# Kernel tuning notes

Hardware: AMD Instinct MI355X
Metric: run time of the kernel (lower is better)

## Reference

```python
import jax, jax.numpy as jnp
import numpy as np

B, T, C = 128, 64, 66
S, L, W = 512, 2, 32  # state_size, num_layers, window_size


def _gru_cell(x, h, Wih, Whh, bih, bhh):
    # PyTorch GRU cell. x:[B,in], h:[B,S]; gate order r,z,n.
    gi = x @ Wih.T + bih  # [B,3S]
    gh = h @ Whh.T + bhh
    ir, iz, inn = jnp.split(gi, 3, axis=-1)
    hr, hz, hn = jnp.split(gh, 3, axis=-1)
    r = jax.nn.sigmoid(ir + hr)
    z = jax.nn.sigmoid(iz + hz)
    n = jnp.tanh(inn + r * hn)
    return (1.0 - z) * n + z * h


def setup_inputs() -> dict:
    key = jax.random.key(0)
    ks = jax.random.split(key, 14)
    sc = 0.02
    inp = {
        'x': jax.random.normal(ks[0], (B, T, C), dtype=jnp.float32),
        'Wih0': jax.random.normal(ks[1], (3 * S, C), dtype=jnp.float32) * sc,
        'Whh0': jax.random.normal(ks[2], (3 * S, S), dtype=jnp.float32) * sc,
        'bih0': jax.random.normal(ks[3], (3 * S,), dtype=jnp.float32) * sc,
        'bhh0': jax.random.normal(ks[4], (3 * S,), dtype=jnp.float32) * sc,
        'Wih1': jax.random.normal(ks[5], (3 * S, S), dtype=jnp.float32) * sc,
        'Whh1': jax.random.normal(ks[6], (3 * S, S), dtype=jnp.float32) * sc,
        'bih1': jax.random.normal(ks[7], (3 * S,), dtype=jnp.float32) * sc,
        'bhh1': jax.random.normal(ks[8], (3 * S,), dtype=jnp.float32) * sc,
        'Wt': jax.random.normal(ks[9], (1, W), dtype=jnp.float32) * sc,   # temporal_fc_last: Linear(W,1)
        'bt': jnp.zeros((1,), dtype=jnp.float32),
        'Ws': jax.random.normal(ks[10], (C, S), dtype=jnp.float32) * sc,  # spatial_fc: Linear(S,C)
        'bs': jnp.zeros((C,), dtype=jnp.float32),
    }
    return inp


def reference(x, Wih0, Whh0, bih0, bhh0, Wih1, Whh1, bih1, bhh1, Wt, bt, Ws, bs):
    Bx, Tx, Cx = x.shape
    h0 = jnp.zeros((Bx, S), dtype=x.dtype)
    h1 = jnp.zeros((Bx, S), dtype=x.dtype)

    def stack_step(h0, h1, xt):
        h0 = _gru_cell(xt, h0, Wih0, Whh0, bih0, bhh0)
        h1 = _gru_cell(h0, h1, Wih1, Whh1, bih1, bhh1)
        return h0, h1

    # ---- encoder over x[:, :-1, :] ----
    def enc_step(carry, xt):
        h0, h1 = stack_step(carry[0], carry[1], xt)
        return (h0, h1), h1

    (h0, h1), enc_out = jax.lax.scan(enc_step, (h0, h1), x[:, :-1, :].transpose(1, 0, 2))
    # enc_out: [T-1, B, S]; sliding window of the last W encoder outputs: [B, W, S]
    window = enc_out[-W:].transpose(1, 0, 2)

    def dec_step(carry, _):
        h0, h1, win, dinp = carry  # dinp: [B, C]
        h0, h1 = stack_step(h0, h1, dinp)
        win = jnp.concatenate([win[:, 1:, :], h1[:, None, :]], axis=1)  # slide window
        # temporal_fc_last over time axis (after b n d -> b d n): [B, S]
        temp = jnp.einsum('bws,w->bs', win, Wt[0]) + bt[0]
        out = temp @ Ws.T + bs  # spatial_fc: [B, C]
        new_frame = out + dinp  # recursive residual
        return (h0, h1, win, new_frame), new_frame

    init = (h0, h1, window, x[:, -1, :])
    _, frames = jax.lax.scan(dec_step, init, None, length=Tx)  # [T, B, C]
    return frames.transpose(1, 0, 2)  # [B, T, C]
```

## Files before the change

kernel.cpp:

```cpp
#include <hip/hip_runtime.h>
#include <stdint.h>

typedef unsigned short u16;
typedef uint32_t u32;
typedef __attribute__((ext_vector_type(8))) short short8;
typedef __attribute__((ext_vector_type(4))) float floatx4;

constexpr int BB = 128;
constexpr int TT = 64;
constexpr int CC = 66;
constexpr int CPAD = 96;
constexpr int SS = 512;
constexpr int NGATE = 1536;
constexpr int NGRP = 8;
constexpr int GBLK = 16;
constexpr int GS = 16 * SS;


__device__ __forceinline__ u16 f2bf(float f) {
    u32 u = __float_as_uint(f);
    u32 r = (u + 0x7fffu + ((u >> 16) & 1u)) >> 16;
    return (u16)r;
}
__device__ __forceinline__ float bf2f(u16 h) {
    return __uint_as_float(((u32)h) << 16);
}
__device__ __forceinline__ float sigm(float x) { return 1.f / (1.f + __expf(-x)); }
__device__ __forceinline__ float tanh_f(float x) { return 1.f - 2.f / (1.f + __expf(2.f * x)); }

__device__ __forceinline__ void store_u16_cc(u16* p, u16 v) {
    asm volatile("global_store_short %0, %1, off sc0 sc1"
                 :: "v"(p), "v"((u32)v) : "memory");
}
__device__ __forceinline__ void load_issue_cc(const u16* p, short8& d) {
    asm volatile("global_load_dwordx4 %0, %1, off sc0 sc1"
                 : "=v"(d) : "v"(p));
}
__device__ __forceinline__ void vm_drain() {
    asm volatile("s_waitcnt vmcnt(0)" ::: "memory");
}

__global__ void prep1_kernel(const float* __restrict__ x,
                             const float* __restrict__ Wih0,
                             const float* __restrict__ Whh0,
                             const float* __restrict__ Wih1,
                             const float* __restrict__ Whh1,
                             const float* __restrict__ Ws,
                             u16* __restrict__ xbf, u16* __restrict__ wi0,
                             u16* __restrict__ wh0, u16* __restrict__ wi1,
                             u16* __restrict__ wh1, u16* __restrict__ wsb)
{
    const int N_xbf = BB * TT * CPAD;
    const int N_wi0 = NGATE * CPAD;
    const int N_whh = NGATE * SS;
    const int N_wsb = 80 * SS;
    const long total = (long)N_xbf + N_wi0 + 3L * N_whh + N_wsb;
    for (long i = (long)blockIdx.x * blockDim.x + threadIdx.x; i < total;
         i += (long)gridDim.x * blockDim.x) {
        long idx = i;
        if (idx < N_xbf) {
            int c = idx % CPAD; int bt = idx / CPAD;
            float v = (c < CC) ? x[(long)bt * CC + c] : 0.f;
            xbf[idx] = f2bf(v); continue;
        }
        idx -= N_xbf;
        if (idx < N_wi0) {
            int c = idx % CPAD; int n = idx / CPAD;
            float v = (c < CC) ? Wih0[(long)n * CC + c] : 0.f;
            wi0[idx] = f2bf(v); continue;
        }
        idx -= N_wi0;
        if (idx < N_whh) { wh0[idx] = f2bf(Whh0[idx]); continue; }
        idx -= N_whh;
        if (idx < N_whh) { wi1[idx] = f2bf(Wih1[idx]); continue; }
        idx -= N_whh;
        if (idx < N_whh) { wh1[idx] = f2bf(Whh1[idx]); continue; }
        idx -= N_whh;
        {
            int s = idx % SS; int c = idx / SS;
            wsb[idx] = (c < CC) ? f2bf(Ws[(long)c * SS + s]) : (u16)0;
        }
    }
}

__global__ void prep2_kernel(const float* __restrict__ x,
                             const float* __restrict__ Wih0,
                             const float* __restrict__ Ws,
                             const float* __restrict__ bs,
                             u16* __restrict__ Mbf, float* __restrict__ c0vec,
                             float* __restrict__ gi0i)
{
    const long NM = (long)NGATE * SS;
    const long NC = NGATE;
    const long NG = (long)BB * NGATE;
    const long total = NM + NC + NG;
    for (long i = (long)blockIdx.x * blockDim.x + threadIdx.x; i < total;
         i += (long)gridDim.x * blockDim.x) {
        long idx = i;
        if (idx < NM) {
            int s = idx % SS; int g = idx / SS;
            float acc = 0.f;
            for (int c = 0; c < CC; ++c)
                acc += Wih0[(long)g * CC + c] * Ws[(long)c * SS + s];
            Mbf[idx] = f2bf(acc); continue;
        }
        idx -= NM;
        if (idx < NC) {
            int g = idx;
            float acc = 0.f;
            for (int c = 0; c < CC; ++c) acc += Wih0[(long)g * CC + c] * bs[c];
            c0vec[g] = acc; continue;
        }
        idx -= NC;
        {
            int g = idx % NGATE; int b = idx / NGATE;
            float acc = 0.f;
            const float* xl = x + ((long)b * TT + (TT - 1)) * CC;
            for (int c = 0; c < CC; ++c) acc += xl[c] * Wih0[(long)g * CC + c];
            gi0i[idx] = acc;
        }
    }
}

__device__ __forceinline__ void load_afrags(const u16* __restrict__ st,
                                            int lane, short8* a) {
#pragma unroll
    for (int kc = 0; kc < 16; ++kc)
        load_issue_cc(st + (long)kc * 512 + lane * 8, a[kc]);
}

#define MFMA_BF16(a, wp, acc) \
    acc = __builtin_amdgcn_mfma_f32_16x16x32_bf16(a, *(const short8*)(wp), acc, 0, 0, 0)

__device__ __forceinline__ void mm3_reg(const short8* a,
                                        const u16* __restrict__ w0,
                                        const u16* __restrict__ w1,
                                        const u16* __restrict__ w2,
                                        floatx4& A0, floatx4& A1, floatx4& A2) {
#pragma unroll
    for (int kc = 0; kc < 16; ++kc) {
        const int k = kc << 5;
        MFMA_BF16(a[kc], w0 + k, A0);
        MFMA_BF16(a[kc], w1 + k, A1);
        MFMA_BF16(a[kc], w2 + k, A2);
    }
}

template <int K>
__device__ __forceinline__ void mm3_g(const u16* __restrict__ aP,
                                      const u16* __restrict__ w0,
                                      const u16* __restrict__ w1,
                                      const u16* __restrict__ w2,
                                      floatx4& A0, floatx4& A1, floatx4& A2) {
#pragma unroll
    for (int k = 0; k < K; k += 32) {
        short8 a = *(const short8*)(aP + k);
        MFMA_BF16(a, w0 + k, A0);
        MFMA_BF16(a, w1 + k, A1);
        MFMA_BF16(a, w2 + k, A2);
    }
}

__device__ __forceinline__ void wait2(const int* __restrict__ f0, int t0,
                                      const int* __restrict__ f1, int t1) {
    const int lane = threadIdx.x & 63;
    const int* p = (lane < 32) ? (f0 + lane) : (f1 + (lane - 32));
    const int tgt = (lane < 32) ? t0 : t1;
    for (;;) {
        int v = __hip_atomic_load(p, __ATOMIC_RELAXED, __HIP_MEMORY_SCOPE_AGENT);
        if (__all(v >= tgt)) break;
        __builtin_amdgcn_s_sleep(1);
    }
    asm volatile("" ::: "memory");
}

__device__ __forceinline__ void set_flag(int* f, int v) {
    if ((threadIdx.x & 63) == 0)
        __hip_atomic_store(f, v, __ATOMIC_RELAXED, __HIP_MEMORY_SCOPE_AGENT);
}

__global__ __launch_bounds__(256, 1) void persist_kernel(
    const u16* __restrict__ xbf,
    const u16* __restrict__ wi0, const u16* __restrict__ wh0,
    const u16* __restrict__ wi1, const u16* __restrict__ wh1,
    const u16* __restrict__ Mbf,
    const float* __restrict__ bih0, const float* __restrict__ bhh0,
    const float* __restrict__ bih1, const float* __restrict__ bhh1,
    const float* __restrict__ c0vec, const float* __restrict__ gi0i,
    const float* __restrict__ Wt, const float* __restrict__ bt,
    u16* __restrict__ h0buf,
    u16* __restrict__ h1buf,
    u16* __restrict__ tstage,
    u16* __restrict__ temps,
    int* __restrict__ gflags)
{
    const int tid = threadIdx.x;
    const int wave = tid >> 6, lane = tid & 63;
    const int l15 = lane & 15, quad = lane >> 4;
    const int grp = blockIdx.x >> 4, rank = blockIdx.x & 15;
    const int b0g = grp * 16;
    const int wsub = wave & 1;
    const int sg = rank * 32 + wsub * 16 + l15;
    const bool l0w = wave < 2;

    const int stoff = ((sg >> 3) << 7) + (sg & 7);

    u16* const h0g = h0buf + (long)grp * 4 * GS;
    u16* const h1g = h1buf + (long)grp * 2 * GS;
    u16* const tsg = tstage + (long)grp * 2 * GS;
    int* const f0 = gflags + grp * 64;
    int* const f1 = f0 + 32;
    const int myflag = rank * 2 + wsub;

    float bir, biz, bin, bhn;
    float c0r = 0.f, c0z = 0.f, c0n = 0.f;
    float hf[4] = {0.f, 0.f, 0.f, 0.f};
    float gi[12];
    float wt[32]; float btv = 0.f;
    u32 wreg[4][16];
#pragma unroll
    for (int r = 0; r < 4; ++r)
#pragma unroll
        for (int i = 0; i < 16; ++i) wreg[r][i] = 0u;

    if (l0w) {
        bir = bih0[sg] + bhh0[sg];
        biz = bih0[512 + sg] + bhh0[512 + sg];
        bin = bih0[1024 + sg];
        bhn = bhh0[1024 + sg];
        c0r = c0vec[sg]; c0z = c0vec[512 + sg]; c0n = c0vec[1024 + sg];
#pragma unroll
        for (int g3 = 0; g3 < 3; ++g3)
#pragma unroll
            for (int r = 0; r < 4; ++r)
                gi[g3 * 4 + r] =
                    gi0i[(long)(b0g + quad * 4 + r) * NGATE + g3 * 512 + sg];
    } else {
        bir = bih1[sg] + bhh1[sg];
        biz = bih1[512 + sg] + bhh1[512 + sg];
        bin = bih1[1024 + sg];
        bhn = bhh1[1024 + sg];
#pragma unroll
        for (int j = 0; j < 32; ++j) wt[j] = Wt[j];
        btv = bt[0];
    }

    const u16 *wiR, *wiZ, *wiN, *whR, *whZ, *whN, *mR, *mZ, *mN;
    if (l0w) {
        wiR = wi0 + (long)sg * CPAD + quad * 8;
        wiZ = wi0 + (long)(512 + sg) * CPAD + quad * 8;
        wiN = wi0 + (long)(1024 + sg) * CPAD + quad * 8;
        whR = wh0 + (long)sg * SS + quad * 8;
        whZ = wh0 + (long)(512 + sg) * SS + quad * 8;
        whN = wh0 + (long)(1024 + sg) * SS + quad * 8;
        mR = Mbf + (long)sg * SS + quad * 8;
        mZ = Mbf + (long)(512 + sg) * SS + quad * 8;
        mN = Mbf + (long)(1024 + sg) * SS + quad * 8;
    } else {
        wiR = wi1 + (long)sg * SS + quad * 8;
        wiZ = wi1 + (long)(512 + sg) * SS + quad * 8;
        wiN = wi1 + (long)(1024 + sg) * SS + quad * 8;
        whR = wh1 + (long)sg * SS + quad * 8;
        whZ = wh1 + (long)(512 + sg) * SS + quad * 8;
        whN = wh1 + (long)(1024 + sg) * SS + quad * 8;
        mR = mZ = mN = nullptr;
    }

    short8 fa[16], fb[16];

    if (l0w) {
        for (int t = 0; t < 63; ++t) {
            wait2(f0, t, f1, t - 3);
            load_afrags(h0g + (long)(t & 3) * GS, lane, fa);
            floatx4 aR = {0,0,0,0}, aZ = aR, aNI = aR, aNH = aR;
            const u16* aP = xbf + ((long)(b0g + l15) * TT + t) * CPAD + quad * 8;
            mm3_g<CPAD>(aP, wiR, wiZ, wiN, aR, aZ, aNI);
            vm_drain();
            mm3_reg(fa, whR, whZ, whN, aR, aZ, aNH);
            u16* dst = h0g + (long)((t + 1) & 3) * GS + stoff;
#pragma unroll
            for (int r = 0; r < 4; ++r) {
                float rr = sigm(aR[r] + bir);
                float zz = sigm(aZ[r] + biz);
                float nn = tanh_f(aNI[r] + bin + rr * (aNH[r] + bhn));
                float hv = (1.f - zz) * nn + zz * hf[r];
                hf[r] = hv;
                store_u16_cc(dst + (quad * 4 + r) * 8, f2bf(hv));
            }
            vm_drain();
            set_flag(f0 + myflag, t + 1);
        }
        for (int d = 0; d < 64; ++d) {
            const int t = 63 + d;
            wait2(f0, t, f1, (d > 0) ? t : 60);
            if (d > 0) {
                load_afrags(tsg + (long)((d - 1) & 1) * GS, lane, fb);
            }
            load_afrags(h0g + (long)(t & 3) * GS, lane, fa);
            vm_drain();
            if (d > 0) {
                floatx4 tR = {0,0,0,0}, tZ = tR, tN = tR;
                mm3_reg(fb, mR, mZ, mN, tR, tZ, tN);
#pragma unroll
                for (int r = 0; r < 4; ++r) {
                    gi[r] += tR[r] + c0r;
                    gi[4 + r] += tZ[r] + c0z;
                    gi[8 + r] += tN[r] + c0n;
                }
            }
            floatx4 hR = {0,0,0,0}, hZ = hR, hN4 = hR;
            mm3_reg(fa, whR, whZ, whN, hR, hZ, hN4);
            u16* dst = h0g + (long)((t + 1) & 3) * GS + stoff;
#pragma unroll
            for (int r = 0; r < 4; ++r) {
                float rr = sigm(gi[r] + hR[r] + bir);
                float zz = sigm(gi[4 + r] + hZ[r] + biz);
                float nn = tanh_f(gi[8 + r] + bin + rr * (hN4[r] + bhn));
                float hv = (1.f - zz) * nn + zz * hf[r];
                hf[r] = hv;
                store_u16_cc(dst + (quad * 4 + r) * 8, f2bf(hv));
            }
            vm_drain();
            set_flag(f0 + myflag, t + 1);
        }
    } else {
        for (int u = 0; u < 63; ++u) {
            wait2(f0, u + 1, f1, u);
            load_afrags(h0g + (long)((u + 1) & 3) * GS, lane, fa);
            load_afrags(h1g + (long)(u & 1) * GS, lane, fb);
            vm_drain();
            floatx4 aR = {0,0,0,0}, aZ = aR, aNI = aR, aNH = aR;
            mm3_reg(fa, wiR, wiZ, wiN, aR, aZ, aNI);
            mm3_reg(fb, whR, whZ, whN, aR, aZ, aNH);
            u16* dst = h1g + (long)((u + 1) & 1) * GS + stoff;
#pragma unroll
            for (int r = 0; r < 4; ++r) {
                float rr = sigm(aR[r] + bir);
                float zz = sigm(aZ[r] + biz);
                float nn = tanh_f(aNI[r] + bin + rr * (aNH[r] + bhn));
                float hv = (1.f - zz) * nn + zz * hf[r];
                hf[r] = hv;
                u16 hb = f2bf(hv);
                store_u16_cc(dst + (quad * 4 + r) * 8, hb);
#pragma unroll
                for (int i = 0; i < 15; ++i)
                    wreg[r][i] = (wreg[r][i] >> 16) | (wreg[r][i + 1] << 16);
                wreg[r][15] = (wreg[r][15] >> 16) | ((u32)hb << 16);
            }
            vm_drain();
            set_flag(f1 + myflag, u + 1);
        }
        for (int d = 0; d < 64; ++d) {
            const int u = 63 + d;
            wait2(f0, u + 1, f1, u);
            load_afrags(h0g + (long)((u + 1) & 3) * GS, lane, fa);
            load_afrags(h1g + (long)(u & 1) * GS, lane, fb);
            vm_drain();
            floatx4 aR = {0,0,0,0}, aZ = aR, aNI = aR, aNH = aR;
            mm3_reg(fa, wiR, wiZ, wiN, aR, aZ, aNI);
            mm3_reg(fb, whR, whZ, whN, aR, aZ, aNH);
            u16* dst = h1g + (long)((u + 1) & 1) * GS + stoff;
            u16* tdst = tsg + (long)(d & 1) * GS + stoff;
            u16* tOut = temps + (long)d * (BB * SS);
#pragma unroll
            for (int r = 0; r < 4; ++r) {
                float rr = sigm(aR[r] + bir);
                float zz = sigm(aZ[r] + biz);
                float nn = tanh_f(aNI[r] + bin + rr * (aNH[r] + bhn));
                float hv = (1.f - zz) * nn + zz * hf[r];
                hf[r] = hv;
                u16 hb = f2bf(hv);
                store_u16_cc(dst + (quad * 4 + r) * 8, hb);
#pragma unroll
                for (int i = 0; i < 15; ++i)
                    wreg[r][i] = (wreg[r][i] >> 16) | (wreg[r][i + 1] << 16);
                wreg[r][15] = (wreg[r][15] >> 16) | ((u32)hb << 16);
                float tacc = btv;
#pragma unroll
                for (int i = 0; i < 16; ++i) {
                    u32 wv = wreg[r][i];
                    tacc += __uint_as_float(wv << 16) * wt[2 * i];
                    tacc += __uint_as_float(wv & 0xffff0000u) * wt[2 * i + 1];
                }
                u16 tb = f2bf(tacc);
                store_u16_cc(tdst + (quad * 4 + r) * 8, tb);
                tOut[(long)(b0g + quad * 4 + r) * SS + sg] = tb;
            }
            vm_drain();
            set_flag(f1 + myflag, u + 1);
        }
    }
}

__global__ __launch_bounds__(256) void frames_kernel(
    const u16* __restrict__ temps, const float* __restrict__ x,
    const u16* __restrict__ wsb, const float* __restrict__ bs,
    float* __restrict__ outp)
{
    const int b = blockIdx.x, tid = threadIdx.x;
    const int wave = tid >> 6, lane = tid & 63;
    const int l15 = lane & 15, quad = lane >> 4;
    __shared__ float P[64][81];

    const int e0 = wave * 16;
    floatx4 acc[5];
#pragma unroll
    for (int ct = 0; ct < 5; ++ct) acc[ct] = (floatx4){0.f, 0.f, 0.f, 0.f};
    const u16* aBase =
        temps + (long)(e0 + l15) * (BB * SS) + (long)b * SS + quad * 8;
#pragma unroll
    for (int kc = 0; kc < 16; ++kc) {
        short8 a = *(const short8*)(aBase + kc * 32);
#pragma unroll
        for (int ct = 0; ct < 5; ++ct) {
            const u16* wp = wsb + (long)(ct * 16 + l15) * SS + quad * 8 + kc * 32;
            MFMA_BF16(a, wp, acc[ct]);
        }
    }
#pragma unroll
    for (int ct = 0; ct < 5; ++ct)
#pragma unroll
        for (int r = 0; r < 4; ++r)
            P[e0 + quad * 4 + r][ct * 16 + l15] = acc[ct][r];
    __syncthreads();

    const int c = tid;
    if (c < CC) {
        float cum = x[((long)b * TT + (TT - 1)) * CC + c];
        const float bsv = bs[c];
        for (int e = 0; e < TT; ++e) {
            cum += P[e][c] + bsv;
            outp[(long)b * TT * CC + (long)e * CC + c] = cum;
        }
    }
}

extern "C" void kernel_launch(void* const* d_in, const int* in_sizes, int n_in,
                              void* d_out, int out_size, void* d_ws, size_t ws_size,
                              hipStream_t stream)
{
    const float* x    = (const float*)d_in[0];
    const float* Wih0 = (const float*)d_in[1];
    const float* Whh0 = (const float*)d_in[2];
    const float* bih0 = (const float*)d_in[3];
    const float* bhh0 = (const float*)d_in[4];
    const float* Wih1 = (const float*)d_in[5];
    const float* Whh1 = (const float*)d_in[6];
    const float* bih1 = (const float*)d_in[7];
    const float* bhh1 = (const float*)d_in[8];
    const float* Wt   = (const float*)d_in[9];
    const float* bt   = (const float*)d_in[10];
    const float* Ws   = (const float*)d_in[11];
    const float* bs   = (const float*)d_in[12];
    float* outp = (float*)d_out;

    char* p = (char*)d_ws;
    auto alloc = [&](size_t bytes) -> char* {
        char* r = p; p += (bytes + 255) & ~(size_t)255; return r;
    };
    u16* h0buf = (u16*)alloc((size_t)NGRP * 4 * GS * 2);
    u16* h1buf = (u16*)alloc((size_t)NGRP * 2 * GS * 2);
    u16* tstage = (u16*)alloc((size_t)NGRP * 2 * GS * 2);
    u16* xbf = (u16*)alloc((size_t)BB * TT * CPAD * 2);
    u16* wi0 = (u16*)alloc((size_t)NGATE * CPAD * 2);
    u16* wh0 = (u16*)alloc((size_t)NGATE * SS * 2);
    u16* wi1 = (u16*)alloc((size_t)NGATE * SS * 2);
    u16* wh1 = (u16*)alloc((size_t)NGATE * SS * 2);
    u16* Mbf = (u16*)alloc((size_t)NGATE * SS * 2);
    u16* wsb = (u16*)alloc((size_t)80 * SS * 2);
    float* c0vec = (float*)alloc((size_t)NGATE * 4);
    float* gi0i  = (float*)alloc((size_t)BB * NGATE * 4);
    u16* temps = (u16*)alloc((size_t)TT * BB * SS * 2);
    int* gflags = (int*)alloc((size_t)NGRP * 64 * 4);

    hipMemsetAsync(h0buf, 0, (size_t)NGRP * 4 * GS * 2, stream);
    hipMemsetAsync(h1buf, 0, (size_t)NGRP * 2 * GS * 2, stream);
    hipMemsetAsync(gflags, 0, (size_t)NGRP * 64 * 4, stream);

    prep1_kernel<<<1024, 256, 0, stream>>>(x, Wih0, Whh0, Wih1, Whh1, Ws,
                                           xbf, wi0, wh0, wi1, wh1, wsb);
    prep2_kernel<<<1024, 256, 0, stream>>>(x, Wih0, Ws, bs, Mbf, c0vec, gi0i);

    persist_kernel<<<NGRP * GBLK, 256, 0, stream>>>(
        xbf, wi0, wh0, wi1, wh1, Mbf, bih0, bhh0, bih1, bhh1,
        c0vec, gi0i, Wt, bt, h0buf, h1buf, tstage, temps, gflags);

    frames_kernel<<<BB, 256, 0, stream>>>(temps, x, wsb, bs, outp);
}
```

Measured before the change: 2.516 ms.

## Coalesce hidden-state stores via LDS staging and split waits to overlap recurrent matmuls

Hidden and temporal values are now staged through shared memory so each wave writes them with one coalesced 8-byte store per lane. Before, each value went out as a separate 2-byte coherent store. The flag waits are also split: layer-1 waves start their own recurrent h1 matmul before waiting on the layer-0 flag. Decoder layer-0 waves do their h0 matmul before waiting for the temporal staging buffer. This shortens the critical-path dependency chain between the layers, at the cost of extra LDS traffic and wave barriers, and it relies on the revised flag ordering being correct.

```diff
diff --git a/kernel.cpp b/kernel.cpp
--- a/kernel.cpp
+++ b/kernel.cpp
@@ -5,6 +5,7 @@
 typedef uint32_t u32;
 typedef __attribute__((ext_vector_type(8))) short short8;
 typedef __attribute__((ext_vector_type(4))) float floatx4;
+typedef __attribute__((ext_vector_type(2))) unsigned int u32x2;
 
 constexpr int BB = 128;
 constexpr int TT = 64;
@@ -28,13 +29,13 @@
 __device__ __forceinline__ float sigm(float x) { return 1.f / (1.f + __expf(-x)); }
 __device__ __forceinline__ float tanh_f(float x) { return 1.f - 2.f / (1.f + __expf(2.f * x)); }
 
-__device__ __forceinline__ void store_u16_cc(u16* p, u16 v) {
-    asm volatile("global_store_short %0, %1, off sc0 sc1"
-                 :: "v"(p), "v"((u32)v) : "memory");
-}
 __device__ __forceinline__ void load_issue_cc(const u16* p, short8& d) {
     asm volatile("global_load_dwordx4 %0, %1, off sc0 sc1"
                  : "=v"(d) : "v"(p));
+}
+__device__ __forceinline__ void store_u64_cc(u16* p, u32x2 v) {
+    asm volatile("global_store_dwordx2 %0, %1, off sc0 sc1"
+                 :: "v"(p), "v"(v) : "memory");
 }
 __device__ __forceinline__ void vm_drain() {
     asm volatile("s_waitcnt vmcnt(0)" ::: "memory");
@@ -174,9 +175,35 @@
     asm volatile("" ::: "memory");
 }
 
+__device__ __forceinline__ void wait1(const int* __restrict__ f, int tgt) {
+    const int lane = threadIdx.x & 63;
+    const int* p = f + (lane & 31);
+    for (;;) {
+        int v = __hip_atomic_load(p, __ATOMIC_RELAXED, __HIP_MEMORY_SCOPE_AGENT);
+        if (__all(v >= tgt)) break;
+        __builtin_amdgcn_s_sleep(1);
+    }
+    asm volatile("" ::: "memory");
+}
+
 __device__ __forceinline__ void set_flag(int* f, int v) {
     if ((threadIdx.x & 63) == 0)
         __hip_atomic_store(f, v, __ATOMIC_RELAXED, __HIP_MEMORY_SCOPE_AGENT);
+}
+
+__device__ __forceinline__ void staged_store(u16* __restrict__ gdst,
+                                             u16* __restrict__ lds,
+                                             const u16 hb[4],
+                                             int l15, int quad, int lane)
+{
+#pragma unroll
+    for (int r = 0; r < 4; ++r)
+        lds[((l15 >> 3) << 7) + ((quad << 2) + r) * 8 + (l15 & 7)] = hb[r];
+    __builtin_amdgcn_wave_barrier();
+    const u32* lp = (const u32*)(lds + (lane << 2));
+    u32x2 v; v[0] = lp[0]; v[1] = lp[1];
+    store_u64_cc(gdst + (lane << 2), v);
+    __builtin_amdgcn_wave_barrier();
 }
 
 __global__ __launch_bounds__(256, 1) void persist_kernel(
@@ -203,7 +230,11 @@
     const int sg = rank * 32 + wsub * 16 + l15;
     const bool l0w = wave < 2;
 
-    const int stoff = ((sg >> 3) << 7) + (sg & 7);
+    __shared__ u16 stg[4][512];
+    u16* const ldsH = &stg[wave][0];
+    u16* const ldsT = &stg[wave][256];
+
+    const int wbase = (rank * 4 + wsub * 2) << 7;
 
     u16* const h0g = h0buf + (long)grp * 4 * GS;
     u16* const h1g = h1buf + (long)grp * 2 * GS;
@@ -277,7 +308,7 @@
             mm3_g<CPAD>(aP, wiR, wiZ, wiN, aR, aZ, aNI);
             vm_drain();
             mm3_reg(fa, whR, whZ, whN, aR, aZ, aNH);
-            u16* dst = h0g + (long)((t + 1) & 3) * GS + stoff;
+            u16 hb[4];
 #pragma unroll
             for (int r = 0; r < 4; ++r) {
                 float rr = sigm(aR[r] + bir);
@@ -285,20 +316,24 @@
                 float nn = tanh_f(aNI[r] + bin + rr * (aNH[r] + bhn));
                 float hv = (1.f - zz) * nn + zz * hf[r];
                 hf[r] = hv;
-                store_u16_cc(dst + (quad * 4 + r) * 8, f2bf(hv));
+                hb[r] = f2bf(hv);
             }
+            staged_store(h0g + (long)((t + 1) & 3) * GS + wbase, ldsH, hb,
+                         l15, quad, lane);
             vm_drain();
             set_flag(f0 + myflag, t + 1);
         }
         for (int d = 0; d < 64; ++d) {
             const int t = 63 + d;
-            wait2(f0, t, f1, (d > 0) ? t : 60);
+            wait2(f0, t, f1, t - 3);
+            load_afrags(h0g + (long)(t & 3) * GS, lane, fa);
+            vm_drain();
+            floatx4 hR = {0,0,0,0}, hZ = hR, hN4 = hR;
+            mm3_reg(fa, whR, whZ, whN, hR, hZ, hN4);
             if (d > 0) {
+                wait1(f1, t);
                 load_afrags(tsg + (long)((d - 1) & 1) * GS, lane, fb);
-            }
-            load_afrags(h0g + (long)(t & 3) * GS, lane, fa);
-            vm_drain();
-            if (d > 0) {
+                vm_drain();
                 floatx4 tR = {0,0,0,0}, tZ = tR, tN = tR;
                 mm3_reg(fb, mR, mZ, mN, tR, tZ, tN);
 #pragma unroll
@@ -308,9 +343,7 @@
                     gi[8 + r] += tN[r] + c0n;
                 }
             }
-            floatx4 hR = {0,0,0,0}, hZ = hR, hN4 = hR;
-            mm3_reg(fa, whR, whZ, whN, hR, hZ, hN4);
-            u16* dst = h0g + (long)((t + 1) & 3) * GS + stoff;
+            u16 hb[4];
 #pragma unroll
             for (int r = 0; r < 4; ++r) {
                 float rr = sigm(gi[r] + hR[r] + bir);
@@ -318,21 +351,25 @@
                 float nn = tanh_f(gi[8 + r] + bin + rr * (hN4[r] + bhn));
                 float hv = (1.f - zz) * nn + zz * hf[r];
                 hf[r] = hv;
-                store_u16_cc(dst + (quad * 4 + r) * 8, f2bf(hv));
+                hb[r] = f2bf(hv);
             }
+            staged_store(h0g + (long)((t + 1) & 3) * GS + wbase, ldsH, hb,
+                         l15, quad, lane);
             vm_drain();
             set_flag(f0 + myflag, t + 1);
         }
     } else {
         for (int u = 0; u < 63; ++u) {
-            wait2(f0, u + 1, f1, u);
+            wait1(f1, u);
+            load_afrags(h1g + (long)(u & 1) * GS, lane, fb);
+            vm_drain();
+            floatx4 aR = {0,0,0,0}, aZ = aR, aNI = aR, aNH = aR;
+            mm3_reg(fb, whR, whZ, whN, aR, aZ, aNH);
+            wait1(f0, u + 1);
             load_afrags(h0g + (long)((u + 1) & 3) * GS, lane, fa);
-            load_afrags(h1g + (long)(u & 1) * GS, lane, fb);
-            vm_drain();
-            floatx4 aR = {0,0,0,0}, aZ = aR, aNI = aR, aNH = aR;
+            vm_drain();
             mm3_reg(fa, wiR, wiZ, wiN, aR, aZ, aNI);
-            mm3_reg(fb, whR, whZ, whN, aR, aZ, aNH);
-            u16* dst = h1g + (long)((u + 1) & 1) * GS + stoff;
+            u16 hb[4];
 #pragma unroll
             for (int r = 0; r < 4; ++r) {
                 float rr = sigm(aR[r] + bir);
@@ -340,28 +377,31 @@
                 float nn = tanh_f(aNI[r] + bin + rr * (aNH[r] + bhn));
                 float hv = (1.f - zz) * nn + zz * hf[r];
                 hf[r] = hv;
-                u16 hb = f2bf(hv);
-                store_u16_cc(dst + (quad * 4 + r) * 8, hb);
+                u16 v = f2bf(hv);
+                hb[r] = v;
 #pragma unroll
                 for (int i = 0; i < 15; ++i)
                     wreg[r][i] = (wreg[r][i] >> 16) | (wreg[r][i + 1] << 16);
-                wreg[r][15] = (wreg[r][15] >> 16) | ((u32)hb << 16);
+                wreg[r][15] = (wreg[r][15] >> 16) | ((u32)v << 16);
             }
+            staged_store(h1g + (long)((u + 1) & 1) * GS + wbase, ldsH, hb,
+                         l15, quad, lane);
             vm_drain();
             set_flag(f1 + myflag, u + 1);
         }
         for (int d = 0; d < 64; ++d) {
             const int u = 63 + d;
-            wait2(f0, u + 1, f1, u);
+            wait1(f1, u);
+            load_afrags(h1g + (long)(u & 1) * GS, lane, fb);
+            vm_drain();
+            floatx4 aR = {0,0,0,0}, aZ = aR, aNI = aR, aNH = aR;
+            mm3_reg(fb, whR, whZ, whN, aR, aZ, aNH);
+            wait1(f0, u + 1);
             load_afrags(h0g + (long)((u + 1) & 3) * GS, lane, fa);
-            load_afrags(h1g + (long)(u & 1) * GS, lane, fb);
-            vm_drain();
-            floatx4 aR = {0,0,0,0}, aZ = aR, aNI = aR, aNH = aR;
+            vm_drain();
             mm3_reg(fa, wiR, wiZ, wiN, aR, aZ, aNI);
-            mm3_reg(fb, whR, whZ, whN, aR, aZ, aNH);
-            u16* dst = h1g + (long)((u + 1) & 1) * GS + stoff;
-            u16* tdst = tsg + (long)(d & 1) * GS + stoff;
             u16* tOut = temps + (long)d * (BB * SS);
+            u16 hb[4], tb4[4];
 #pragma unroll
             for (int r = 0; r < 4; ++r) {
                 float rr = sigm(aR[r] + bir);
@@ -369,12 +409,12 @@
                 float nn = tanh_f(aNI[r] + bin + rr * (aNH[r] + bhn));
                 float hv = (1.f - zz) * nn + zz * hf[r];
                 hf[r] = hv;
-                u16 hb = f2bf(hv);
-                store_u16_cc(dst + (quad * 4 + r) * 8, hb);
+                u16 v = f2bf(hv);
+                hb[r] = v;
 #pragma unroll
                 for (int i = 0; i < 15; ++i)
                     wreg[r][i] = (wreg[r][i] >> 16) | (wreg[r][i + 1] << 16);
-                wreg[r][15] = (wreg[r][15] >> 16) | ((u32)hb << 16);
+                wreg[r][15] = (wreg[r][15] >> 16) | ((u32)v << 16);
                 float tacc = btv;
 #pragma unroll
                 for (int i = 0; i < 16; ++i) {
@@ -383,9 +423,13 @@
                     tacc += __uint_as_float(wv & 0xffff0000u) * wt[2 * i + 1];
                 }
                 u16 tb = f2bf(tacc);
-                store_u16_cc(tdst + (quad * 4 + r) * 8, tb);
+                tb4[r] = tb;
                 tOut[(long)(b0g + quad * 4 + r) * SS + sg] = tb;
             }
+            staged_store(h1g + (long)((u + 1) & 1) * GS + wbase, ldsH, hb,
+                         l15, quad, lane);
+            staged_store(tsg + (long)(d & 1) * GS + wbase, ldsT, tb4,
+                         l15, quad, lane);
             vm_drain();
             set_flag(f1 + myflag, u + 1);
         }
```

Measured after the change: 2.480 ms. Within noise of the previous version (-1.4%).
